# Kernel optimization log

Measured on AMD Instinct MI355X. Metric: run time of the kernel, lower is better.

The kernel has to match this reference:

```python
import jax, jax.numpy as jnp
import numpy as np

NUM_HEADS = 16


def setup_inputs() -> dict:
    key = jax.random.key(0)
    k1, k2, k3, k4 = jax.random.split(key, 4)
    B, S, E = 2, 2048, 1024
    x = jax.random.normal(k1, (B, S, E), dtype=jnp.float32)
    src_padding_mask = jax.random.randint(k2, (B, S), 0, 2) > 0  # True = keep
    # xavier-uniform-ish scale for linear weights (shape (out, in), torch convention)
    w_qkv = jax.random.normal(k3, (3 * E, E), dtype=jnp.float32) * (1.0 / np.sqrt(E))
    w_o = jax.random.normal(k4, (E, E), dtype=jnp.float32) * (1.0 / np.sqrt(E))
    return {"x": x, "src_padding_mask": src_padding_mask, "w_qkv": w_qkv, "w_o": w_o}


def reference(x, src_padding_mask, w_qkv, w_o):
    B, S, E = x.shape
    H = NUM_HEADS
    D = E // H
    # fused qkv projection: (B,S,3E) -> (B,S,H,3D) -> split
    qkv = jnp.einsum("bse,fe->bsf", x, w_qkv).reshape(B, S, H, 3 * D)
    q, k, v = jnp.split(qkv, 3, axis=-1)
    # (B,H,S,D)
    q = q.transpose(0, 2, 1, 3)
    k = k.transpose(0, 2, 1, 3)
    v = v.transpose(0, 2, 1, 3)
    logits = jnp.einsum("bhqd,bhkd->bhqk", q, k) / jnp.sqrt(jnp.float32(D))
    logits = jnp.where(src_padding_mask[:, None, None, :], logits, -jnp.inf)
    attn = jax.nn.softmax(logits, axis=-1)
    values = jnp.einsum("bhqk,bhkd->bhqd", attn, v)  # (B,H,S,D)
    values = values.transpose(0, 2, 1, 3).reshape(B, S, E)
    out = jnp.einsum("bse,fe->bsf", values, w_o)
    return out
```

## Files before the change

### kernel.cpp

```cpp
#include <hip/hip_runtime.h>
#include <hip/hip_bf16.h>

#define B_NUM 2
#define S_LEN 2048
#define E_DIM 1024
#define H_NUM 16
#define D_DIM 64
#define QKV_LD 3072
#define QSCALE_LOG2E 0.18033688011112042f

typedef __attribute__((ext_vector_type(8))) short bf16x8;
typedef __attribute__((ext_vector_type(8))) unsigned short u16x8;
typedef __attribute__((ext_vector_type(4))) unsigned short u16x4;
typedef __attribute__((ext_vector_type(4))) float f32x4;
typedef __attribute__((ext_vector_type(16))) float f32x16;
typedef __attribute__((ext_vector_type(2))) int i32x2;

static __device__ __forceinline__ unsigned short f2bf(float f) {
    union { float f; unsigned int u; } v; v.f = f;
    unsigned int r = v.u + 0x7fffu + ((v.u >> 16) & 1u);
    return (unsigned short)(r >> 16);
}

static __device__ __forceinline__ unsigned cvtpk_bf16(float lo, float hi) {
    unsigned r;
    asm("v_cvt_pk_bf16_f32 %0, %1, %2" : "=v"(r) : "v"(lo), "v"(hi));
    return r;
}

static __device__ __forceinline__ void gload16(const void* gsrc, void* ldst) {
    __builtin_amdgcn_global_load_lds(
        (const __attribute__((address_space(1))) unsigned int*)gsrc,
        (__attribute__((address_space(3))) unsigned int*)ldst, 16, 0, 0);
}

__global__ __launch_bounds__(256)
void cvt_f32_bf16(const float* __restrict__ in, unsigned short* __restrict__ outp, int n4) {
    int i = blockIdx.x * blockDim.x + threadIdx.x;
    if (i < n4) {
        float4 f = ((const float4*)in)[i];
        u16x4 o = { f2bf(f.x), f2bf(f.y), f2bf(f.z), f2bf(f.w) };
        ((u16x4*)outp)[i] = o;
    }
}

template <bool OUT_BF16, bool QSCALE>
__global__ __launch_bounds__(256)
void gemm_bt_mfma128(const unsigned short* __restrict__ A,
                     const unsigned short* __restrict__ Bw,
                     void* __restrict__ Cv, int M, int N, int K) {
    __shared__ unsigned short As[128 * 64];
    __shared__ unsigned short Bs[128 * 64];
    char* const AsB = (char*)As;
    char* const BsB = (char*)Bs;
    const int tid  = threadIdx.x;
    const int lane = tid & 63;
    const int w    = tid >> 6;
    const int lg   = lane >> 4;
    const int lq   = lane & 15;
    const int bm = blockIdx.y * 128;
    const int bn = blockIdx.x * 128;
    const int wr = (w >> 1) * 64;
    const int wc = (w & 1) * 64;
    const int lrow8 = lane >> 3;
    const int gblk  = (lane & 7) ^ lrow8;

    f32x4 acc[4][4];
#pragma unroll
    for (int i = 0; i < 4; ++i)
#pragma unroll
        for (int j = 0; j < 4; ++j) acc[i][j] = (f32x4){0.f, 0.f, 0.f, 0.f};

    for (int k0 = 0; k0 < K; k0 += 64) {
        __syncthreads();
#pragma unroll
        for (int t = 0; t < 4; ++t) {
            const int c = w * 4 + t;
            const int row = c * 8 + lrow8;
            gload16(A + (size_t)(bm + row) * K + k0 + gblk * 8, AsB + c * 1024);
            gload16(Bw + (size_t)(bn + row) * K + k0 + gblk * 8, BsB + c * 1024);
        }
        __syncthreads();

        bf16x8 af[4][2], bfr[4][2];
#pragma unroll
        for (int rt = 0; rt < 4; ++rt) {
            const int row = wr + rt * 16 + lq;
            const int sz = (row & 7) << 4;
            af[rt][0] = *(const bf16x8*)(AsB + row * 128 + ((lg * 16)      ^ sz));
            af[rt][1] = *(const bf16x8*)(AsB + row * 128 + ((64 + lg * 16) ^ sz));
        }
#pragma unroll
        for (int ct = 0; ct < 4; ++ct) {
            const int row = wc + ct * 16 + lq;
            const int sz = (row & 7) << 4;
            bfr[ct][0] = *(const bf16x8*)(BsB + row * 128 + ((lg * 16)      ^ sz));
            bfr[ct][1] = *(const bf16x8*)(BsB + row * 128 + ((64 + lg * 16) ^ sz));
        }
#pragma unroll
        for (int rt = 0; rt < 4; ++rt)
#pragma unroll
            for (int ct = 0; ct < 4; ++ct) {
                acc[rt][ct] = __builtin_amdgcn_mfma_f32_16x16x32_bf16(af[rt][0], bfr[ct][0], acc[rt][ct], 0, 0, 0);
                acc[rt][ct] = __builtin_amdgcn_mfma_f32_16x16x32_bf16(af[rt][1], bfr[ct][1], acc[rt][ct], 0, 0, 0);
            }
    }

#pragma unroll
    for (int rt = 0; rt < 4; ++rt)
#pragma unroll
        for (int ct = 0; ct < 4; ++ct) {
            const int row = bm + wr + rt * 16 + lg * 4;
            const int col = bn + wc + ct * 16 + lq;
            float scale = 1.f;
            if constexpr (QSCALE) scale = ((col % 192) < 64) ? QSCALE_LOG2E : 1.f;
#pragma unroll
            for (int r = 0; r < 4; ++r) {
                float vv = acc[rt][ct][r] * scale;
                if constexpr (OUT_BF16)
                    ((unsigned short*)Cv)[(size_t)(row + r) * N + col] = f2bf(vv);
                else
                    ((float*)Cv)[(size_t)(row + r) * N + col] = vv;
            }
        }
}

template <bool OUT_BF16, bool QSCALE>
__global__ __launch_bounds__(256)
void gemm_bt_mfma(const unsigned short* __restrict__ A,
                  const unsigned short* __restrict__ Bw,
                  void* __restrict__ Cv, int M, int N, int K) {
    __shared__ unsigned short As[64 * 64];
    __shared__ unsigned short Bs[64 * 64];
    char* const AsB = (char*)As;
    char* const BsB = (char*)Bs;
    const int tid  = threadIdx.x;
    const int lane = tid & 63;
    const int w    = tid >> 6;
    const int lg   = lane >> 4;
    const int lq   = lane & 15;
    const int bm = blockIdx.y * 64;
    const int bn = blockIdx.x * 64;
    const int wr = (w >> 1) * 32;
    const int wc = (w & 1) * 32;
    const int sr = tid >> 2;
    const int sc = (tid & 3) * 16;
    const int swzS = (sr & 7) << 4;

    f32x4 acc[2][2];
#pragma unroll
    for (int i = 0; i < 2; ++i)
#pragma unroll
        for (int j = 0; j < 2; ++j) acc[i][j] = (f32x4){0.f, 0.f, 0.f, 0.f};

    const unsigned short* ap = A  + (size_t)(bm + sr) * K + sc;
    const unsigned short* bp = Bw + (size_t)(bn + sr) * K + sc;

    for (int k0 = 0; k0 < K; k0 += 64) {
        __syncthreads();
        u16x8 av0 = *(const u16x8*)(ap + k0);
        u16x8 av1 = *(const u16x8*)(ap + k0 + 8);
        u16x8 bv0 = *(const u16x8*)(bp + k0);
        u16x8 bv1 = *(const u16x8*)(bp + k0 + 8);
        *(u16x8*)(AsB + sr * 128 + ((sc * 2)      ^ swzS)) = av0;
        *(u16x8*)(AsB + sr * 128 + ((sc * 2 + 16) ^ swzS)) = av1;
        *(u16x8*)(BsB + sr * 128 + ((sc * 2)      ^ swzS)) = bv0;
        *(u16x8*)(BsB + sr * 128 + ((sc * 2 + 16) ^ swzS)) = bv1;
        __syncthreads();

        bf16x8 af[2][2], bfr[2][2];
#pragma unroll
        for (int rt = 0; rt < 2; ++rt) {
            const int row = wr + rt * 16 + lq;
            const int sz = (row & 7) << 4;
            af[rt][0] = *(const bf16x8*)(AsB + row * 128 + ((lg * 16)      ^ sz));
            af[rt][1] = *(const bf16x8*)(AsB + row * 128 + ((64 + lg * 16) ^ sz));
        }
#pragma unroll
        for (int ct = 0; ct < 2; ++ct) {
            const int row = wc + ct * 16 + lq;
            const int sz = (row & 7) << 4;
            bfr[ct][0] = *(const bf16x8*)(BsB + row * 128 + ((lg * 16)      ^ sz));
            bfr[ct][1] = *(const bf16x8*)(BsB + row * 128 + ((64 + lg * 16) ^ sz));
        }
#pragma unroll
        for (int rt = 0; rt < 2; ++rt)
#pragma unroll
            for (int ct = 0; ct < 2; ++ct) {
                acc[rt][ct] = __builtin_amdgcn_mfma_f32_16x16x32_bf16(af[rt][0], bfr[ct][0], acc[rt][ct], 0, 0, 0);
                acc[rt][ct] = __builtin_amdgcn_mfma_f32_16x16x32_bf16(af[rt][1], bfr[ct][1], acc[rt][ct], 0, 0, 0);
            }
    }

#pragma unroll
    for (int rt = 0; rt < 2; ++rt)
#pragma unroll
        for (int ct = 0; ct < 2; ++ct) {
            const int row = bm + wr + rt * 16 + lg * 4;
            const int col = bn + wc + ct * 16 + lq;
            float scale = 1.f;
            if constexpr (QSCALE) scale = ((col % 192) < 64) ? QSCALE_LOG2E : 1.f;
#pragma unroll
            for (int r = 0; r < 4; ++r) {
                float vv = acc[rt][ct][r] * scale;
                if constexpr (OUT_BF16)
                    ((unsigned short*)Cv)[(size_t)(row + r) * N + col] = f2bf(vv);
                else
                    ((float*)Cv)[(size_t)(row + r) * N + col] = vv;
            }
        }
}

__global__ __launch_bounds__(256)
void attn_v8(const unsigned short* __restrict__ qkv, const int* __restrict__ mask,
             unsigned short* __restrict__ vout) {
    __shared__ __align__(16) char pool[32768];
    __shared__ __align__(16) float BiasF[S_LEN];
    __shared__ float RsM[2][2][32];

    const int tid  = threadIdx.x;
    const int lane = tid & 63;
    const int w    = tid >> 6;
    const int ln   = lane & 31;
    const int hi   = lane >> 5;
    const int qh   = w >> 1;
    const int kh   = w & 1;

    const int d0  = blockIdx.x + 16 * blockIdx.y + 256 * blockIdx.z;
    const int lin = (d0 & 7) * 64 + (d0 >> 3);
    const int q0 = (lin & 15) * 128;
    const int h  = (lin >> 4) & 15;
    const int b  = lin >> 8;
    const unsigned short* const kv =
        qkv + (size_t)b * S_LEN * QKV_LD + (size_t)h * (3 * D_DIM);

    char* const poolK = pool;
    char* const poolV = pool + 16384;

    {
        const int4* mr = (const int4*)(mask + (size_t)b * S_LEN);
        int4 m0 = mr[tid * 2];
        int4 m1 = mr[tid * 2 + 1];
        float4 f0 = { m0.x ? 0.f : -30000.f, m0.y ? 0.f : -30000.f,
                      m0.z ? 0.f : -30000.f, m0.w ? 0.f : -30000.f };
        float4 f1 = { m1.x ? 0.f : -30000.f, m1.y ? 0.f : -30000.f,
                      m1.z ? 0.f : -30000.f, m1.w ? 0.f : -30000.f };
        ((float4*)BiasF)[tid * 2]     = f0;
        ((float4*)BiasF)[tid * 2 + 1] = f1;
    }

    bf16x8 qf[2][4];
#pragma unroll
    for (int qs = 0; qs < 2; ++qs) {
        const unsigned short* qp = kv + (size_t)(q0 + qh * 64 + qs * 32 + ln) * QKV_LD + hi * 8;
#pragma unroll
        for (int kk = 0; kk < 4; ++kk)
            qf[qs][kk] = *(const bf16x8*)(qp + kk * 16);
    }

    const int lrow8 = lane >> 3;
    const int gblk  = (lane & 7) ^ lrow8;
    const int vkb = (tid & 15) * 4;
    const int vdb = (tid >> 4) * 4;

    {
#pragma unroll
        for (int t = 0; t < 2; ++t) {
            const int c = w * 2 + t;
            gload16(kv + (size_t)(c * 8 + lrow8) * QKV_LD + D_DIM + gblk * 8,
                    poolK + c * 1024);
        }
        u16x4 vr[4];
#pragma unroll
        for (int i = 0; i < 4; ++i)
            vr[i] = *(const u16x4*)(kv + (size_t)(vkb + i) * QKV_LD + 2 * D_DIM + vdb);
#pragma unroll
        for (int j = 0; j < 4; ++j) {
            u16x4 o = { vr[0][j], vr[1][j], vr[2][j], vr[3][j] };
            const int row = vdb + j;
            *(u16x4*)(poolV + row * 128 + ((vkb * 2) ^ ((row & 7) << 4))) = o;
        }
    }
    __syncthreads();

    f32x16 accO[2][2];
#pragma unroll
    for (int dt = 0; dt < 2; ++dt)
#pragma unroll
        for (int qs = 0; qs < 2; ++qs)
#pragma unroll
            for (int r = 0; r < 16; ++r) accO[dt][qs][r] = 0.f;
    f32x4 rsv[2] = {(f32x4){0.f, 0.f, 0.f, 0.f}, (f32x4){0.f, 0.f, 0.f, 0.f}};

    const int NT = S_LEN / 64;
    const int krow = kh * 32 + ln;
    const int kswz = (ln & 7) << 4;
    for (int it = 0; it < NT; ++it) {
        const int cur = it & 1;
        const int kv0 = it * 64;
        char* const KsC = poolK + cur * 8192;
        char* const VtC = poolV + cur * 8192;
        const bool pf = (it + 1 < NT);

        u16x4 vr[4];
        if (pf) {
            const int kvn = kv0 + 64;
#pragma unroll
            for (int t = 0; t < 2; ++t) {
                const int c = w * 2 + t;
                gload16(kv + (size_t)(kvn + c * 8 + lrow8) * QKV_LD + D_DIM + gblk * 8,
                        poolK + (cur ^ 1) * 8192 + c * 1024);
            }
#pragma unroll
            for (int i = 0; i < 4; ++i)
                vr[i] = *(const u16x4*)(kv + (size_t)(kvn + vkb + i) * QKV_LD + 2 * D_DIM + vdb);
        }

        bf16x8 kf[4];
#pragma unroll
        for (int kk = 0; kk < 4; ++kk)
            kf[kk] = *(const bf16x8*)(KsC + krow * 128 + (((kk * 16 + hi * 8) * 2) ^ kswz));

        f32x16 s[2];
#pragma unroll
        for (int m = 0; m < 4; ++m) {
            f32x4 b4 = *(const f32x4*)(&BiasF[kv0 + kh * 32 + m * 8 + hi * 4]);
#pragma unroll
            for (int i = 0; i < 4; ++i) { s[0][m * 4 + i] = b4[i]; s[1][m * 4 + i] = b4[i]; }
        }

        __builtin_amdgcn_s_setprio(1);
#pragma unroll
        for (int kk = 0; kk < 4; ++kk) {
            s[0] = __builtin_amdgcn_mfma_f32_32x32x16_bf16(kf[kk], qf[0][kk], s[0], 0, 0, 0);
            s[1] = __builtin_amdgcn_mfma_f32_32x32x16_bf16(kf[kk], qf[1][kk], s[1], 0, 0, 0);
        }
        __builtin_amdgcn_s_setprio(0);

#pragma unroll
        for (int qs = 0; qs < 2; ++qs)
#pragma unroll
            for (int r = 0; r < 16; ++r) {
                float p = __builtin_amdgcn_exp2f(s[qs][r]);
                s[qs][r] = p;
                rsv[qs][r & 3] += p;
            }

        bf16x8 pb[2][2];
#pragma unroll
        for (int qs = 0; qs < 2; ++qs) {
            unsigned wA[4], wB[4];
#pragma unroll
            for (int m = 0; m < 4; ++m) {
                wA[m] = cvtpk_bf16(s[qs][4 * m + 0], s[qs][4 * m + 1]);
                wB[m] = cvtpk_bf16(s[qs][4 * m + 2], s[qs][4 * m + 3]);
            }
#pragma unroll
            for (int t = 0; t < 2; ++t) {
                i32x2 ra = __builtin_amdgcn_permlane32_swap((int)wA[2 * t], (int)wA[2 * t + 1], false, false);
                i32x2 rb = __builtin_amdgcn_permlane32_swap((int)wB[2 * t], (int)wB[2 * t + 1], false, false);
                union { unsigned u[4]; bf16x8 v; } uu;
                uu.u[0] = (unsigned)ra[0];
                uu.u[1] = (unsigned)rb[0];
                uu.u[2] = (unsigned)ra[1];
                uu.u[3] = (unsigned)rb[1];
                pb[qs][t] = uu.v;
            }
        }

        __builtin_amdgcn_s_setprio(1);
#pragma unroll
        for (int dt = 0; dt < 2; ++dt) {
            const int drow = dt * 32 + ln;
            const int swz = (ln & 7) << 4;
#pragma unroll
            for (int t = 0; t < 2; ++t) {
                const int n = 2 * kh + t;
                bf16x8 va = *(const bf16x8*)(VtC + drow * 128 + (((n * 16 + hi * 8) * 2) ^ swz));
                accO[dt][0] = __builtin_amdgcn_mfma_f32_32x32x16_bf16(va, pb[0][t], accO[dt][0], 0, 0, 0);
                accO[dt][1] = __builtin_amdgcn_mfma_f32_32x32x16_bf16(va, pb[1][t], accO[dt][1], 0, 0, 0);
            }
        }
        __builtin_amdgcn_s_setprio(0);

        if (pf) {
#pragma unroll
            for (int j = 0; j < 4; ++j) {
                u16x4 o = { vr[0][j], vr[1][j], vr[2][j], vr[3][j] };
                const int row = vdb + j;
                *(u16x4*)(poolV + (cur ^ 1) * 8192 + row * 128 + ((vkb * 2) ^ ((row & 7) << 4))) = o;
            }
        }
        __syncthreads();
    }

    float rs[2];
#pragma unroll
    for (int qs = 0; qs < 2; ++qs) {
        float t = rsv[qs][0] + rsv[qs][1] + rsv[qs][2] + rsv[qs][3];
        i32x2 rr = __builtin_amdgcn_permlane32_swap(__float_as_int(t), __float_as_int(t), false, false);
        rs[qs] = __int_as_float(rr[0]) + __int_as_float(rr[1]);
    }

    __syncthreads();
    const int lswz = (lane & 7) << 4;
    if (kh == 1) {
        char* const reg = pool + qh * 16384;
#pragma unroll
        for (int qs = 0; qs < 2; ++qs) {
#pragma unroll
            for (int dt = 0; dt < 2; ++dt)
#pragma unroll
                for (int r4 = 0; r4 < 4; ++r4) {
                    f32x4 v = { accO[dt][qs][4 * r4 + 0], accO[dt][qs][4 * r4 + 1],
                                accO[dt][qs][4 * r4 + 2], accO[dt][qs][4 * r4 + 3] };
                    *(f32x4*)(reg + lane * 256 + ((qs * 128 + dt * 64 + r4 * 16) ^ lswz)) = v;
                }
            if (hi == 0) RsM[qh][qs][ln] = rs[qs];
        }
    }
    __syncthreads();
    if (kh == 0) {
        const char* const reg = pool + qh * 16384;
#pragma unroll
        for (int qs = 0; qs < 2; ++qs) {
            const float inv = 1.f / (rs[qs] + RsM[qh][qs][ln]);
            unsigned short* op = vout +
                (size_t)(b * S_LEN + q0 + qh * 64 + qs * 32 + ln) * E_DIM + h * D_DIM;
#pragma unroll
            for (int dt = 0; dt < 2; ++dt)
#pragma unroll
                for (int m = 0; m < 4; ++m) {
                    f32x4 part = *(const f32x4*)(reg + lane * 256 + ((qs * 128 + dt * 64 + m * 16) ^ lswz));
                    u16x4 o;
#pragma unroll
                    for (int i = 0; i < 4; ++i)
                        o[i] = f2bf((accO[dt][qs][4 * m + i] + part[i]) * inv);
                    *(u16x4*)(op + dt * 32 + m * 8 + hi * 4) = o;
                }
        }
    }
}

extern "C" void kernel_launch(void* const* d_in, const int* in_sizes, int n_in,
                              void* d_out, int out_size, void* d_ws, size_t ws_size,
                              hipStream_t stream) {
    const float* x      = (const float*)d_in[0];
    const int*   mask   = (const int*)d_in[1];
    const float* w_qkv  = (const float*)d_in[2];
    const float* w_o    = (const float*)d_in[3];
    float*       out    = (float*)d_out;

    const int M = B_NUM * S_LEN;
    unsigned short* qkvb = (unsigned short*)d_ws;
    unsigned short* vbuf = qkvb + (size_t)M * 3 * E_DIM;
    unsigned short* xb   = vbuf + (size_t)M * E_DIM;
    unsigned short* wqb  = xb   + (size_t)M * E_DIM;
    unsigned short* wob  = wqb  + (size_t)3 * E_DIM * E_DIM;

    dim3 blk(256);
    {
        int n4;
        n4 = M * E_DIM / 4;
        cvt_f32_bf16<<<dim3((n4 + 255) / 256), blk, 0, stream>>>(x, xb, n4);
        n4 = 3 * E_DIM * E_DIM / 4;
        cvt_f32_bf16<<<dim3((n4 + 255) / 256), blk, 0, stream>>>(w_qkv, wqb, n4);
        n4 = E_DIM * E_DIM / 4;
        cvt_f32_bf16<<<dim3((n4 + 255) / 256), blk, 0, stream>>>(w_o, wob, n4);
    }

    gemm_bt_mfma128<true, true><<<dim3(3 * E_DIM / 128, M / 128), blk, 0, stream>>>(
        xb, wqb, qkvb, M, 3 * E_DIM, E_DIM);

    attn_v8<<<dim3(S_LEN / 128, H_NUM, B_NUM), blk, 0, stream>>>(qkvb, mask, vbuf);

    gemm_bt_mfma<false, false><<<dim3(E_DIM / 64, M / 64), blk, 0, stream>>>(
        vbuf, wob, out, M, E_DIM, E_DIM);
}
```

Baseline: 129.3 us.

## Load K directly into registers and give each wave a private V transpose buffer

The attention loop no longer shares double-buffered K/V tiles in LDS across the block. Each wave loads its K fragments straight from global memory into registers and transposes its own 32-key V slice into a per-wave LDS region, which removes the per-iteration block barrier. This trades shared-tile reuse and software prefetch for independent wave progress. The price is duplicated global/L2 traffic across the two query-half waves and load latency exposed inside the loop.

```diff
diff --git a/kernel.cpp b/kernel.cpp
--- a/kernel.cpp
+++ b/kernel.cpp
@@ -212,8 +212,8 @@
 }
 
 __global__ __launch_bounds__(256)
-void attn_v8(const unsigned short* __restrict__ qkv, const int* __restrict__ mask,
-             unsigned short* __restrict__ vout) {
+void attn_v10(const unsigned short* __restrict__ qkv, const int* __restrict__ mask,
+              unsigned short* __restrict__ vout) {
     __shared__ __align__(16) char pool[32768];
     __shared__ __align__(16) float BiasF[S_LEN];
     __shared__ float RsM[2][2][32];
@@ -233,9 +233,6 @@
     const int b  = lin >> 8;
     const unsigned short* const kv =
         qkv + (size_t)b * S_LEN * QKV_LD + (size_t)h * (3 * D_DIM);
-
-    char* const poolK = pool;
-    char* const poolV = pool + 16384;
 
     {
         const int4* mr = (const int4*)(mask + (size_t)b * S_LEN);
@@ -258,30 +255,11 @@
             qf[qs][kk] = *(const bf16x8*)(qp + kk * 16);
     }
 
-    const int lrow8 = lane >> 3;
-    const int gblk  = (lane & 7) ^ lrow8;
-    const int vkb = (tid & 15) * 4;
-    const int vdb = (tid >> 4) * 4;
-
-    {
-#pragma unroll
-        for (int t = 0; t < 2; ++t) {
-            const int c = w * 2 + t;
-            gload16(kv + (size_t)(c * 8 + lrow8) * QKV_LD + D_DIM + gblk * 8,
-                    poolK + c * 1024);
-        }
-        u16x4 vr[4];
-#pragma unroll
-        for (int i = 0; i < 4; ++i)
-            vr[i] = *(const u16x4*)(kv + (size_t)(vkb + i) * QKV_LD + 2 * D_DIM + vdb);
-#pragma unroll
-        for (int j = 0; j < 4; ++j) {
-            u16x4 o = { vr[0][j], vr[1][j], vr[2][j], vr[3][j] };
-            const int row = vdb + j;
-            *(u16x4*)(poolV + row * 128 + ((vkb * 2) ^ ((row & 7) << 4))) = o;
-        }
-    }
     __syncthreads();
+
+    const int kgrp = lane & 7;
+    const int dgrp = lane >> 3;
+    char* const myV = pool + w * 8192;
 
     f32x16 accO[2][2];
 #pragma unroll
@@ -293,33 +271,26 @@
     f32x4 rsv[2] = {(f32x4){0.f, 0.f, 0.f, 0.f}, (f32x4){0.f, 0.f, 0.f, 0.f}};
 
     const int NT = S_LEN / 64;
-    const int krow = kh * 32 + ln;
-    const int kswz = (ln & 7) << 4;
     for (int it = 0; it < NT; ++it) {
-        const int cur = it & 1;
         const int kv0 = it * 64;
-        char* const KsC = poolK + cur * 8192;
-        char* const VtC = poolV + cur * 8192;
-        const bool pf = (it + 1 < NT);
-
-        u16x4 vr[4];
-        if (pf) {
-            const int kvn = kv0 + 64;
-#pragma unroll
-            for (int t = 0; t < 2; ++t) {
-                const int c = w * 2 + t;
-                gload16(kv + (size_t)(kvn + c * 8 + lrow8) * QKV_LD + D_DIM + gblk * 8,
-                        poolK + (cur ^ 1) * 8192 + c * 1024);
-            }
+
+        u16x8 vr[4];
+        {
+            const unsigned short* vp = kv + (size_t)(kv0 + kh * 32 + kgrp * 4) * QKV_LD
+                                          + 2 * D_DIM + dgrp * 8;
 #pragma unroll
             for (int i = 0; i < 4; ++i)
-                vr[i] = *(const u16x4*)(kv + (size_t)(kvn + vkb + i) * QKV_LD + 2 * D_DIM + vdb);
+                vr[i] = *(const u16x8*)(vp + (size_t)i * QKV_LD);
         }
 
         bf16x8 kf[4];
-#pragma unroll
-        for (int kk = 0; kk < 4; ++kk)
-            kf[kk] = *(const bf16x8*)(KsC + krow * 128 + (((kk * 16 + hi * 8) * 2) ^ kswz));
+        {
+            const unsigned short* kp = kv + (size_t)(kv0 + kh * 32 + ln) * QKV_LD
+                                          + D_DIM + hi * 8;
+#pragma unroll
+            for (int kk = 0; kk < 4; ++kk)
+                kf[kk] = *(const bf16x8*)(kp + kk * 16);
+        }
 
         f32x16 s[2];
 #pragma unroll
@@ -368,30 +339,27 @@
             }
         }
 
+#pragma unroll
+        for (int j = 0; j < 8; ++j) {
+            u16x4 o = { vr[0][j], vr[1][j], vr[2][j], vr[3][j] };
+            const int row = dgrp * 8 + j;
+            *(u16x4*)(myV + row * 128
+                      + ((((kgrp >> 1) ^ (row & 7)) << 4) + ((kgrp & 1) * 8))) = o;
+        }
+
         __builtin_amdgcn_s_setprio(1);
 #pragma unroll
         for (int dt = 0; dt < 2; ++dt) {
             const int drow = dt * 32 + ln;
-            const int swz = (ln & 7) << 4;
 #pragma unroll
             for (int t = 0; t < 2; ++t) {
-                const int n = 2 * kh + t;
-                bf16x8 va = *(const bf16x8*)(VtC + drow * 128 + (((n * 16 + hi * 8) * 2) ^ swz));
+                const int c = t * 2 + hi;
+                bf16x8 va = *(const bf16x8*)(myV + drow * 128 + ((c ^ (drow & 7)) << 4));
                 accO[dt][0] = __builtin_amdgcn_mfma_f32_32x32x16_bf16(va, pb[0][t], accO[dt][0], 0, 0, 0);
                 accO[dt][1] = __builtin_amdgcn_mfma_f32_32x32x16_bf16(va, pb[1][t], accO[dt][1], 0, 0, 0);
             }
         }
         __builtin_amdgcn_s_setprio(0);
-
-        if (pf) {
-#pragma unroll
-            for (int j = 0; j < 4; ++j) {
-                u16x4 o = { vr[0][j], vr[1][j], vr[2][j], vr[3][j] };
-                const int row = vdb + j;
-                *(u16x4*)(poolV + (cur ^ 1) * 8192 + row * 128 + ((vkb * 2) ^ ((row & 7) << 4))) = o;
-            }
-        }
-        __syncthreads();
     }
 
     float rs[2];
@@ -472,7 +440,7 @@
     gemm_bt_mfma128<true, true><<<dim3(3 * E_DIM / 128, M / 128), blk, 0, stream>>>(
         xb, wqb, qkvb, M, 3 * E_DIM, E_DIM);
 
-    attn_v8<<<dim3(S_LEN / 128, H_NUM, B_NUM), blk, 0, stream>>>(qkvb, mask, vbuf);
+    attn_v10<<<dim3(S_LEN / 128, H_NUM, B_NUM), blk, 0, stream>>>(qkvb, mask, vbuf);
 
     gemm_bt_mfma<false, false><<<dim3(E_DIM / 64, M / 64), blk, 0, stream>>>(
         vbuf, wob, out, M, E_DIM, E_DIM);
```

New measurement: 128.8 us. About the same (-0.4%).
